# Optimization experiments

Hardware: AMD Instinct MI355X
Metric: run time of the kernel (lower is better)

Reference implementation:

```python
import jax, jax.numpy as jnp
from jax import lax
import numpy as np

NBC, NAC, KF, RHO = 14, 45, 52, 0.05
KT = np.arange(0.8, 0, -1.0 / 64, dtype=np.float32)[None, :]  # (1, 52) AC kernel time axis
K = KT.shape[1]


def _sigm(x, off, slope):
    return jax.nn.sigmoid(slope * (x - off))


def _ac_kernel(log_tr, log_td, kt):
    tr = jnp.exp(log_tr)[:, None]  # (nAC,1)
    td = jnp.exp(log_td)[:, None]
    k = jnp.exp(-kt / td) - jnp.exp(-(td + tr) / (td * tr) * kt)  # (nAC,K)
    return k / jnp.linalg.norm(k, axis=1, keepdims=True)


def setup_inputs() -> dict:
    key = jax.random.key(0)
    ks = jax.random.split(key, 12)
    B, T = 64, 4096
    n = 0.01  # noise_init_scale
    return {
        "x": jax.random.normal(ks[0], (B, T), jnp.float32) * 0.5,
        "bc_kernels": jax.random.normal(ks[1], (NBC, KF), jnp.float32) * 0.1,
        "log_sigmoid_slope": jnp.log(2.0) + n * jax.random.normal(ks[2], (NBC,), jnp.float32),
        "sigmoid_offset": 1.5 + n * jax.random.normal(ks[3], (NBC,), jnp.float32),
        "log_bc_ac_weight": jnp.log(1.0 / NBC) + n * jax.random.normal(ks[4], (NAC, NBC), jnp.float32),
        "log_ac_tau_rise": jnp.log(0.1) + n * jax.random.normal(ks[5], (NAC,), jnp.float32),
        "log_ac_tau_decay": jnp.log(0.1) + n * jax.random.normal(ks[6], (NAC,), jnp.float32),
        "log_ac_sigmoid_slope": jnp.log(2.0) + n * jax.random.normal(ks[7], (NAC,), jnp.float32),
        "ac_sigmoid_offset": 1.5 + n * jax.random.normal(ks[8], (NAC,), jnp.float32),
        "log_ac_bc_weight": jnp.log(0.01) + n * jax.random.normal(ks[9], (NBC, NAC), jnp.float32),
        "out_scale": jnp.ones((NBC,), jnp.float32),
    }


def reference(x, bc_kernels, log_sigmoid_slope, sigmoid_offset, log_bc_ac_weight,
              log_ac_tau_rise, log_ac_tau_decay, log_ac_sigmoid_slope,
              ac_sigmoid_offset, log_ac_bc_weight, out_scale):
    B, T = x.shape
    kt = jnp.asarray(KT)
    # linear_filter: causal conv of stimulus with per-BC kernels -> (T, B, nBC)
    xf = lax.conv_general_dilated(x[:, None, :], bc_kernels[:, None, :], (1,), [(KF - 1, 0)])
    xf = jnp.transpose(xf, (2, 0, 1))  # (T, B, nBC)

    slope = jnp.exp(log_sigmoid_slope)
    ac_slope = jnp.exp(log_ac_sigmoid_slope)
    bc_ac_w = jnp.exp(log_bc_ac_weight)          # (nAC, nBC)
    ac_bc_w = -jnp.exp(log_ac_bc_weight)         # (nBC, nAC)
    ack = _ac_kernel(log_ac_tau_rise, log_ac_tau_decay, kt)  # (nAC, K)

    # --- plain LNR branch (no feedback) ---
    prob_lnr = _sigm(xf, sigmoid_offset, slope)

    def lnr_step(pool, p):
        pool2 = pool + (1.0 - pool) * RHO
        rel = p * pool2
        return pool2 - rel, rel

    _, rel_lnr = lax.scan(lnr_step, jnp.ones((B, NBC), x.dtype), prob_lnr)
    y_lnr = (out_scale * rel_lnr).transpose(1, 0, 2)  # (B, T, nBC)

    # --- BCN branch with AC feedback recurrence ---
    def bcn_step(carry, xt):
        pool, prev_rel, buf = carry
        # append previous release (track_release[i-1]) to sliding window (oldest first)
        buf = jnp.concatenate([buf[..., 1:], prev_rel[..., None]], axis=-1)  # (B, nBC, K)
        drive = jnp.einsum('ak,ab,nbk->na', ack, bc_ac_w, buf)               # (B, nAC)
        ac_out = _sigm(drive, ac_sigmoid_offset, ac_slope)
        fb = ac_out @ ac_bc_w.T                                              # (B, nBC)
        prob = _sigm(xt + fb, sigmoid_offset, slope)
        pool2 = pool + (1.0 - pool) * RHO
        rel = prob * pool2
        return (pool2 - rel, rel, buf), (rel, fb, ac_out)

    init = (jnp.ones((B, NBC), x.dtype), jnp.zeros((B, NBC), x.dtype), jnp.zeros((B, NBC, K), x.dtype))
    _, (rel, fb, ac_out) = lax.scan(bcn_step, init, xf)
    y_bcn = (out_scale * rel).transpose(1, 0, 2)  # (B, T, nBC)
    return y_bcn, fb.transpose(1, 0, 2), ac_out.transpose(1, 0, 2), y_lnr
```

## Files before the change

### kernel.cpp

```cpp
#include <hip/hip_runtime.h>
#include <hip/hip_fp16.h>

#define NBC 14
#define NAC 45
#define KF  52
#define RHO 0.05f
#define TT  4096
#define BB  64
#define CHC 64
#define WU  44
#define NPAIR 32
#define NTW (WU + CHC)
#define SPAN (WU + 2*CHC)
#define XPAD 176
#define LOG2E 1.44269504f
#define XF_BYTES ((size_t)BB * NBC * TT * 2)

typedef float f2 __attribute__((ext_vector_type(2)));
typedef int   i2v __attribute__((ext_vector_type(2)));

__device__ __forceinline__ __half2 bch(unsigned u) { return __builtin_bit_cast(__half2, u); }
__device__ __forceinline__ unsigned bcu(__half2 h) { return __builtin_bit_cast(unsigned, h); }
__device__ __forceinline__ __half2 pk2(float lo, float hi) {
  return __floats2half2_rn(lo, hi);
}
__device__ __forceinline__ __half2 xsum16h(__half2 v) {
#if __has_builtin(__builtin_amdgcn_permlane16_swap)
  i2v r = __builtin_amdgcn_permlane16_swap((int)bcu(v), (int)bcu(v), false, false);
  return __hadd2(bch((unsigned)r[0]), bch((unsigned)r[1]));
#else
  return __hadd2(v, bch((unsigned)__builtin_amdgcn_ds_swizzle((int)bcu(v), (16 << 10) | 0x1f)));
#endif
}
__device__ __forceinline__ __half2 xsum32h(__half2 v) {
#if __has_builtin(__builtin_amdgcn_permlane32_swap)
  i2v r = __builtin_amdgcn_permlane32_swap((int)bcu(v), (int)bcu(v), false, false);
  return __hadd2(bch((unsigned)r[0]), bch((unsigned)r[1]));
#else
  return __hadd2(v, bch((unsigned)__shfl_xor((int)bcu(v), 32)));
#endif
}
__device__ __forceinline__ float exp2_f(float x) {
#if __has_builtin(__builtin_amdgcn_exp2f)
  return __builtin_amdgcn_exp2f(x);
#else
  return exp2f(x);
#endif
}

__global__ __launch_bounds__(256)
void conv_kernel(const float* __restrict__ x, const float* __restrict__ bck,
                 __half* __restrict__ xfg) {
  __shared__ float xs[256 + KF];
  const int tid  = threadIdx.x;
  const int b    = blockIdx.x >> 4;
  const int t0   = (blockIdx.x & 15) << 8;
  for (int i = tid; i < 256 + KF - 1; i += 256) {
    int gt = t0 - (KF - 1) + i;
    xs[i] = (gt >= 0) ? x[b * TT + gt] : 0.f;
  }
  __syncthreads();
  float acc[NBC];
#pragma unroll
  for (int c = 0; c < NBC; ++c) acc[c] = 0.f;
#pragma unroll 4
  for (int k = 0; k < KF; ++k) {
    float xv = xs[tid + k];
#pragma unroll
    for (int c = 0; c < NBC; ++c) acc[c] = fmaf(bck[c * KF + k], xv, acc[c]);
  }
#pragma unroll
  for (int c = 0; c < NBC; ++c)
    xfg[((size_t)b * NBC + c) * TT + t0 + tid] = __float2half(acc[c]);
}

#define POOL_BYTES 6144

template<bool PRECONV>
__global__ __launch_bounds__(64)
void bcn_kernel(const float* __restrict__ x,
                const float* __restrict__ bck,
                const float* __restrict__ lss,
                const float* __restrict__ soff,
                const float* __restrict__ lbaw,
                const float* __restrict__ ltr,
                const float* __restrict__ ltd,
                const float* __restrict__ lass,
                const float* __restrict__ asoff,
                const float* __restrict__ labw,
                const float* __restrict__ oscale,
                const __half* __restrict__ xfg,
                float* __restrict__ out)
{
  __shared__ __align__(16) char pool[POOL_BYTES];
  __half*   xf_lds = (__half*)pool;
  unsigned* acr    = (unsigned*)(pool + 4928);
  unsigned* relr   = (unsigned*)(pool + 5184);
  float*    x_lds  = (float*)(pool + 5248);

  const int lid   = threadIdx.x;
  const int c16   = lid & 15;
  const int q     = lid >> 4;
  const float rowm = (q & 1) ? 0.f : 1.f;
  const int blk   = blockIdx.x;
  const int b     = blk >> 5;
  const int p     = blk & 31;
  const int t0A   = p * (2 * CHC);
  const int t_begin = t0A - WU;

  if constexpr (PRECONV) {
    const __half* src = xfg + (size_t)b * NBC * TT;
    if (p == 0) {
      for (int e = lid; e < NBC * SPAN; e += 64) {
        int c = e / SPAN, i = e - c * SPAN;
        int gt = t_begin + i; if (gt < 0) gt = 0;
        xf_lds[c * XPAD + i] = src[(size_t)c * TT + gt];
      }
    } else {
      for (int c = 0; c < NBC; ++c) {
        if (lid < SPAN / 4) {
          uint2 v = *(const uint2*)(src + (size_t)c * TT + t_begin + 4 * lid);
          *(uint2*)&xf_lds[c * XPAD + 4 * lid] = v;
        }
      }
    }
  } else {
    for (int i = lid; i < SPAN + KF - 1; i += 64) {
      int gt = t_begin - (KF - 1) + i;
      x_lds[i] = (gt >= 0) ? x[b * TT + gt] : 0.f;
    }
    __syncthreads();
    for (int ib = 0; ib < 3; ++ib) {
      int tau = lid + (ib << 6);
      if (tau < SPAN) {
        float acc[NBC];
#pragma unroll
        for (int c = 0; c < NBC; ++c) acc[c] = 0.f;
#pragma unroll 4
        for (int k = 0; k < KF; ++k) {
          float xv = x_lds[tau + k];
#pragma unroll
          for (int c = 0; c < NBC; ++c) acc[c] = fmaf(bck[c * KF + k], xv, acc[c]);
        }
#pragma unroll
        for (int c = 0; c < NBC; ++c) xf_lds[c * XPAD + tau] = __float2half(acc[c]);
      }
    }
    __syncthreads();
  }

  if (lid < 64) acr[lid] = 0u;
  if (lid < 16) relr[lid] = 0u;

  float slope2 = 0.f, soff2 = 0.f, osc_c = 0.f;
  f2 poolP; poolP.x = 1.f; poolP.y = 1.f;
  f2 SA; SA.x = 0.f; SA.y = 0.f;
  f2 SB; SB.x = 0.f; SB.y = 0.f;
  f2 rv2, cn2; rv2.x = rv2.y = cn2.x = cn2.y = 0.f;
  float Adrv2 = 0.f, Boff2 = 0.f;
  __half2 wfbh[16];
  __half2 wuh[NBC];
  f2 yst[8], fst[8];
  unsigned acst[8];

#pragma unroll
  for (int j = 0; j < 16; ++j) wfbh[j] = pk2(0.f, 0.f);
#pragma unroll
  for (int c = 0; c < NBC; ++c) wuh[c] = pk2(0.f, 0.f);

  if (c16 < NBC) {
    float sl = expf(lss[c16]);
    slope2 = sl * LOG2E;
    soff2  = soff[c16] * sl * LOG2E;
    osc_c  = oscale[c16];
#pragma unroll
    for (int j = 0; j < 16; ++j) {
      int a = 16 * q + j;
      if (a < NAC) { float w = -expf(labw[c16 * NAC + a]); wfbh[j] = pk2(w, w); }
    }
  }
  if (lid < NAC) {
    float tr = expf(ltr[lid]);
    float td = expf(ltd[lid]);
    float a1 = 1.f / td;
    float gg = (td + tr) / (td * tr);
    rv2.x = expf(-a1 * 0.015625f);  rv2.y = expf(-gg * 0.015625f);
    cn2.x = expf(-a1 * 0.003125f);  cn2.y = expf(-gg * 0.003125f);
    float nrm = 0.f;
    for (int k = 0; k < KF; ++k) {
      float kt = 0.8f - (float)k * 0.015625f;
      float d = expf(-a1 * kt) - expf(-gg * kt);
      nrm = fmaf(d, d, nrm);
    }
    float inorm  = 1.f / sqrtf(nrm);
    float aslope = expf(lass[lid]);
    Adrv2 = aslope * inorm * LOG2E;
    Boff2 = aslope * asoff[lid] * LOG2E;
#pragma unroll
    for (int c = 0; c < NBC; ++c) {
      float w = expf(lbaw[lid * NBC + c]);
      wuh[c] = pk2(w, w);
    }
  }

  float* yb  = out;
  float* fbp = out + (size_t)BB * TT * NBC;
  float* acp = out + 2 * (size_t)BB * TT * NBC;
  float* ylp = out + 2 * (size_t)BB * TT * NBC + (size_t)BB * TT * NAC;

  __syncthreads();

  auto step = [&](int slot, float xfA, float xfB, bool emit)
      __attribute__((always_inline)) {
    float mzA = fmaf(-Adrv2, SA.x - SA.y, Boff2);
    float mzB = fmaf(-Adrv2, SB.x - SB.y, Boff2);
    float acA = __fdividef(1.f, 1.f + exp2_f(mzA));
    float acB = __fdividef(1.f, 1.f + exp2_f(mzB));
    if (lid < NAC) acr[lid] = bcu(pk2(acA, acB));

    const uint4* ab = (const uint4*)(acr + (q << 4));
    uint4 A0 = ab[0], A1 = ab[1], A2 = ab[2], A3 = ab[3];
    __half2 g0 = __hmul2(wfbh[0], bch(A0.x));
    __half2 g1 = __hmul2(wfbh[1], bch(A0.y));
    g0 = __hfma2(wfbh[2],  bch(A0.z), g0);  g1 = __hfma2(wfbh[3],  bch(A0.w), g1);
    g0 = __hfma2(wfbh[4],  bch(A1.x), g0);  g1 = __hfma2(wfbh[5],  bch(A1.y), g1);
    g0 = __hfma2(wfbh[6],  bch(A1.z), g0);  g1 = __hfma2(wfbh[7],  bch(A1.w), g1);
    g0 = __hfma2(wfbh[8],  bch(A2.x), g0);  g1 = __hfma2(wfbh[9],  bch(A2.y), g1);
    g0 = __hfma2(wfbh[10], bch(A2.z), g0);  g1 = __hfma2(wfbh[11], bch(A2.w), g1);
    g0 = __hfma2(wfbh[12], bch(A3.x), g0);  g1 = __hfma2(wfbh[13], bch(A3.y), g1);
    g0 = __hfma2(wfbh[14], bch(A3.z), g0);  g1 = __hfma2(wfbh[15], bch(A3.w), g1);
    __half2 gs = xsum32h(xsum16h(__hadd2(g0, g1)));
    float fbA = __low2float(gs), fbB = __high2float(gs);

    float mA = fmaf(-slope2, fmaf(rowm, fbA, xfA), soff2);
    float mB = fmaf(-slope2, fmaf(rowm, fbB, xfB), soff2);
    f2 pv;
    pv.x = __fdividef(1.f, 1.f + exp2_f(mA));
    pv.y = __fdividef(1.f, 1.f + exp2_f(mB));
    f2 p2 = poolP * (1.f - RHO) + RHO;
    f2 relP = pv * p2;
    poolP = p2 - relP;
    if (lid < NBC) relr[lid] = bcu(pk2(relP.x, relP.y));
    if (emit) {
      yst[slot] = relP * osc_c;
      f2 t; t.x = fbA; t.y = fbB; fst[slot] = t;
      acst[slot] = bcu(pk2(acA, acB));
    }

    const uint4* rb = (const uint4*)relr;
    uint4 R0 = rb[0], R1 = rb[1], R2 = rb[2], R3 = rb[3];
    __half2 h0 = __hmul2(wuh[0], bch(R0.x));
    __half2 h1 = __hmul2(wuh[1], bch(R0.y));
    h0 = __hfma2(wuh[2],  bch(R0.z), h0);  h1 = __hfma2(wuh[3],  bch(R0.w), h1);
    h0 = __hfma2(wuh[4],  bch(R1.x), h0);  h1 = __hfma2(wuh[5],  bch(R1.y), h1);
    h0 = __hfma2(wuh[6],  bch(R1.z), h0);  h1 = __hfma2(wuh[7],  bch(R1.w), h1);
    h0 = __hfma2(wuh[8],  bch(R2.x), h0);  h1 = __hfma2(wuh[9],  bch(R2.y), h1);
    h0 = __hfma2(wuh[10], bch(R2.z), h0);  h1 = __hfma2(wuh[11], bch(R2.w), h1);
    h0 = __hfma2(wuh[12], bch(R3.x), h0);  h1 = __hfma2(wuh[13], bch(R3.y), h1);
    __half2 uh = __hadd2(h0, h1);
    SA = SA * rv2 + cn2 * __low2float(uh);
    SB = SB * rv2 + cn2 * __high2float(uh);
  };

  auto group = [&](int s4, int slotbase, bool emit) __attribute__((always_inline)) {
    uint2 xa = *(const uint2*)&xf_lds[c16 * XPAD + s4];
    uint2 xb = *(const uint2*)&xf_lds[c16 * XPAD + s4 + CHC];
    __half2 xA01 = bch(xa.x), xA23 = bch(xa.y);
    __half2 xB01 = bch(xb.x), xB23 = bch(xb.y);
    step(slotbase + 0, __low2float(xA01),  __low2float(xB01),  emit);
    step(slotbase + 1, __high2float(xA01), __high2float(xB01), emit);
    step(slotbase + 2, __low2float(xA23),  __low2float(xB23),  emit);
    step(slotbase + 3, __high2float(xA23), __high2float(xB23), emit);
  };

  for (int s4 = 0; s4 < WU; s4 += 4) group(s4, 0, false);

  if (p == 0) {
    SA.x = 0.f; SA.y = 0.f;
    poolP.x = 1.f;
  }

  for (int s8 = WU; s8 < NTW; s8 += 8) {
    group(s8, 0, true);
    group(s8 + 4, 4, true);

    int tg = t0A + (s8 - WU);
    size_t base = (size_t)b * TT + tg;
    if (lid < NBC) {
      size_t ob = base * NBC + lid;
#pragma unroll
      for (int sl = 0; sl < 8; ++sl) {
        yb [ob + sl * NBC]                     = yst[sl].x;
        yb [ob + (size_t)CHC * NBC + sl * NBC] = yst[sl].y;
        fbp[ob + sl * NBC]                     = fst[sl].x;
        fbp[ob + (size_t)CHC * NBC + sl * NBC] = fst[sl].y;
      }
    } else if (lid >= 16 && lid < 16 + NBC) {
      size_t ob = base * NBC + (lid - 16);
#pragma unroll
      for (int sl = 0; sl < 8; ++sl) {
        ylp[ob + sl * NBC]                     = yst[sl].x;
        ylp[ob + (size_t)CHC * NBC + sl * NBC] = yst[sl].y;
      }
    }
    if (lid < NAC) {
      size_t oa = base * NAC + lid;
#pragma unroll
      for (int sl = 0; sl < 8; ++sl) {
        __half2 h = bch(acst[sl]);
        acp[oa + sl * NAC]                     = __low2float(h);
        acp[oa + (size_t)CHC * NAC + sl * NAC] = __high2float(h);
      }
    }
  }
}

extern "C" void kernel_launch(void* const* d_in, const int* in_sizes, int n_in,
                              void* d_out, int out_size, void* d_ws, size_t ws_size,
                              hipStream_t stream) {
  (void)in_sizes; (void)n_in; (void)out_size;
  const float* x    = (const float*)d_in[0];
  const float* bck  = (const float*)d_in[1];
  if (ws_size >= XF_BYTES) {
    __half* xfg = (__half*)d_ws;
    conv_kernel<<<dim3(BB * 16), dim3(256), 0, stream>>>(x, bck, xfg);
    bcn_kernel<true><<<dim3(BB * NPAIR), dim3(64), 0, stream>>>(
        x, bck, (const float*)d_in[2], (const float*)d_in[3], (const float*)d_in[4],
        (const float*)d_in[5], (const float*)d_in[6], (const float*)d_in[7],
        (const float*)d_in[8], (const float*)d_in[9], (const float*)d_in[10],
        xfg, (float*)d_out);
  } else {
    bcn_kernel<false><<<dim3(BB * NPAIR), dim3(64), 0, stream>>>(
        x, bck, (const float*)d_in[2], (const float*)d_in[3], (const float*)d_in[4],
        (const float*)d_in[5], (const float*)d_in[6], (const float*)d_in[7],
        (const float*)d_in[8], (const float*)d_in[9], (const float*)d_in[10],
        (const __half*)nullptr, (float*)d_out);
  }
}
```

Baseline: 92.74 us.

## Replace LDS exchange in recurrence with DPP row rotations

```diff
diff --git a/kernel.cpp b/kernel.cpp
--- a/kernel.cpp
+++ b/kernel.cpp
@@ -24,6 +24,11 @@
 __device__ __forceinline__ __half2 pk2(float lo, float hi) {
   return __floats2half2_rn(lo, hi);
 }
+template<int J>
+__device__ __forceinline__ __half2 rot2(__half2 v) {
+  return __builtin_bit_cast(__half2, __builtin_amdgcn_update_dpp(
+      0, __builtin_bit_cast(int, v), 0x120 + J, 0xF, 0xF, true));
+}
 __device__ __forceinline__ __half2 xsum16h(__half2 v) {
 #if __has_builtin(__builtin_amdgcn_permlane16_swap)
   i2v r = __builtin_amdgcn_permlane16_swap((int)bcu(v), (int)bcu(v), false, false);
@@ -46,6 +51,9 @@
 #else
   return exp2f(x);
 #endif
+}
+__device__ __forceinline__ float sigm(float m) {
+  return __fdividef(1.f, 1.f + exp2_f(m));
 }
 
 __global__ __launch_bounds__(256)
@@ -74,7 +82,7 @@
     xfg[((size_t)b * NBC + c) * TT + t0 + tid] = __float2half(acc[c]);
 }
 
-#define POOL_BYTES 6144
+#define POOL_BYTES 5824
 
 template<bool PRECONV>
 __global__ __launch_bounds__(64)
@@ -93,20 +101,21 @@
                 float* __restrict__ out)
 {
   __shared__ __align__(16) char pool[POOL_BYTES];
-  __half*   xf_lds = (__half*)pool;
-  unsigned* acr    = (unsigned*)(pool + 4928);
-  unsigned* relr   = (unsigned*)(pool + 5184);
-  float*    x_lds  = (float*)(pool + 5248);
+  __half* xf_lds = (__half*)pool;
+  float*  x_lds  = (float*)(pool + 4928);
 
   const int lid   = threadIdx.x;
   const int c16   = lid & 15;
   const int q     = lid >> 4;
-  const float rowm = (q & 1) ? 0.f : 1.f;
+  const int crow  = (c16 < NBC) ? c16 : 0;
   const int blk   = blockIdx.x;
   const int b     = blk >> 5;
   const int p     = blk & 31;
   const int t0A   = p * (2 * CHC);
   const int t_begin = t0A - WU;
+
+  const int probe = __builtin_amdgcn_update_dpp(0, c16, 0x121, 0xF, 0xF, true);
+  const int delta = (c16 - probe) & 15;
 
   if constexpr (PRECONV) {
     const __half* src = xfg + (size_t)b * NBC * TT;
@@ -149,33 +158,29 @@
     __syncthreads();
   }
 
-  if (lid < 64) acr[lid] = 0u;
-  if (lid < 16) relr[lid] = 0u;
-
   float slope2 = 0.f, soff2 = 0.f, osc_c = 0.f;
-  f2 poolP; poolP.x = 1.f; poolP.y = 1.f;
+  f2 poolA; poolA.x = 1.f; poolA.y = 1.f;
+  f2 poolB; poolB.x = 1.f; poolB.y = 1.f;
   f2 SA; SA.x = 0.f; SA.y = 0.f;
   f2 SB; SB.x = 0.f; SB.y = 0.f;
   f2 rv2, cn2; rv2.x = rv2.y = cn2.x = cn2.y = 0.f;
   float Adrv2 = 0.f, Boff2 = 0.f;
   __half2 wfbh[16];
-  __half2 wuh[NBC];
-  f2 yst[8], fst[8];
+  __half2 wuh[16];
+  f2 yst[8], fst[8], lst[8];
   unsigned acst[8];
 
 #pragma unroll
-  for (int j = 0; j < 16; ++j) wfbh[j] = pk2(0.f, 0.f);
-#pragma unroll
-  for (int c = 0; c < NBC; ++c) wuh[c] = pk2(0.f, 0.f);
+  for (int j = 0; j < 16; ++j) { wfbh[j] = pk2(0.f, 0.f); wuh[j] = pk2(0.f, 0.f); }
 
   if (c16 < NBC) {
     float sl = expf(lss[c16]);
     slope2 = sl * LOG2E;
     soff2  = soff[c16] * sl * LOG2E;
     osc_c  = oscale[c16];
-#pragma unroll
     for (int j = 0; j < 16; ++j) {
-      int a = 16 * q + j;
+      int srcl = (c16 - delta * j) & 15;
+      int a = 16 * q + srcl;
       if (a < NAC) { float w = -expf(labw[c16 * NAC + a]); wfbh[j] = pk2(w, w); }
     }
   }
@@ -196,10 +201,9 @@
     float aslope = expf(lass[lid]);
     Adrv2 = aslope * inorm * LOG2E;
     Boff2 = aslope * asoff[lid] * LOG2E;
-#pragma unroll
-    for (int c = 0; c < NBC; ++c) {
-      float w = expf(lbaw[lid * NBC + c]);
-      wuh[c] = pk2(w, w);
+    for (int j = 0; j < 16; ++j) {
+      int srcl = (c16 - delta * j) & 15;
+      if (srcl < NBC) { float w = expf(lbaw[lid * NBC + srcl]); wuh[j] = pk2(w, w); }
     }
   }
 
@@ -214,57 +218,74 @@
       __attribute__((always_inline)) {
     float mzA = fmaf(-Adrv2, SA.x - SA.y, Boff2);
     float mzB = fmaf(-Adrv2, SB.x - SB.y, Boff2);
-    float acA = __fdividef(1.f, 1.f + exp2_f(mzA));
-    float acB = __fdividef(1.f, 1.f + exp2_f(mzB));
-    if (lid < NAC) acr[lid] = bcu(pk2(acA, acB));
-
-    const uint4* ab = (const uint4*)(acr + (q << 4));
-    uint4 A0 = ab[0], A1 = ab[1], A2 = ab[2], A3 = ab[3];
-    __half2 g0 = __hmul2(wfbh[0], bch(A0.x));
-    __half2 g1 = __hmul2(wfbh[1], bch(A0.y));
-    g0 = __hfma2(wfbh[2],  bch(A0.z), g0);  g1 = __hfma2(wfbh[3],  bch(A0.w), g1);
-    g0 = __hfma2(wfbh[4],  bch(A1.x), g0);  g1 = __hfma2(wfbh[5],  bch(A1.y), g1);
-    g0 = __hfma2(wfbh[6],  bch(A1.z), g0);  g1 = __hfma2(wfbh[7],  bch(A1.w), g1);
-    g0 = __hfma2(wfbh[8],  bch(A2.x), g0);  g1 = __hfma2(wfbh[9],  bch(A2.y), g1);
-    g0 = __hfma2(wfbh[10], bch(A2.z), g0);  g1 = __hfma2(wfbh[11], bch(A2.w), g1);
-    g0 = __hfma2(wfbh[12], bch(A3.x), g0);  g1 = __hfma2(wfbh[13], bch(A3.y), g1);
-    g0 = __hfma2(wfbh[14], bch(A3.z), g0);  g1 = __hfma2(wfbh[15], bch(A3.w), g1);
+    float acA = sigm(mzA);
+    float acB = sigm(mzB);
+    __half2 ach = pk2(acA, acB);
+
+    __half2 g0 = __hmul2(wfbh[0], ach);
+    __half2 g1 = __hmul2(wfbh[1], rot2<1>(ach));
+    g0 = __hfma2(wfbh[2],  rot2<2>(ach),  g0);
+    g1 = __hfma2(wfbh[3],  rot2<3>(ach),  g1);
+    g0 = __hfma2(wfbh[4],  rot2<4>(ach),  g0);
+    g1 = __hfma2(wfbh[5],  rot2<5>(ach),  g1);
+    g0 = __hfma2(wfbh[6],  rot2<6>(ach),  g0);
+    g1 = __hfma2(wfbh[7],  rot2<7>(ach),  g1);
+    g0 = __hfma2(wfbh[8],  rot2<8>(ach),  g0);
+    g1 = __hfma2(wfbh[9],  rot2<9>(ach),  g1);
+    g0 = __hfma2(wfbh[10], rot2<10>(ach), g0);
+    g1 = __hfma2(wfbh[11], rot2<11>(ach), g1);
+    g0 = __hfma2(wfbh[12], rot2<12>(ach), g0);
+    g1 = __hfma2(wfbh[13], rot2<13>(ach), g1);
+    g0 = __hfma2(wfbh[14], rot2<14>(ach), g0);
+    g1 = __hfma2(wfbh[15], rot2<15>(ach), g1);
     __half2 gs = xsum32h(xsum16h(__hadd2(g0, g1)));
     float fbA = __low2float(gs), fbB = __high2float(gs);
 
-    float mA = fmaf(-slope2, fmaf(rowm, fbA, xfA), soff2);
-    float mB = fmaf(-slope2, fmaf(rowm, fbB, xfB), soff2);
-    f2 pv;
-    pv.x = __fdividef(1.f, 1.f + exp2_f(mA));
-    pv.y = __fdividef(1.f, 1.f + exp2_f(mB));
-    f2 p2 = poolP * (1.f - RHO) + RHO;
-    f2 relP = pv * p2;
-    poolP = p2 - relP;
-    if (lid < NBC) relr[lid] = bcu(pk2(relP.x, relP.y));
+    float mlA = fmaf(-slope2, xfA, soff2);
+    float mpA = fmaf(-slope2, fbA, mlA);
+    float mlB = fmaf(-slope2, xfB, soff2);
+    float mpB = fmaf(-slope2, fbB, mlB);
+    f2 pvA, pvB;
+    pvA.x = sigm(mpA);  pvA.y = sigm(mlA);
+    pvB.x = sigm(mpB);  pvB.y = sigm(mlB);
+    f2 p2A = poolA * (1.f - RHO) + RHO;
+    f2 p2B = poolB * (1.f - RHO) + RHO;
+    f2 relA = pvA * p2A, relB = pvB * p2B;
+    poolA = p2A - relA;  poolB = p2B - relB;
+    __half2 relh = pk2(relA.x, relB.x);
+
     if (emit) {
-      yst[slot] = relP * osc_c;
-      f2 t; t.x = fbA; t.y = fbB; fst[slot] = t;
-      acst[slot] = bcu(pk2(acA, acB));
-    }
-
-    const uint4* rb = (const uint4*)relr;
-    uint4 R0 = rb[0], R1 = rb[1], R2 = rb[2], R3 = rb[3];
-    __half2 h0 = __hmul2(wuh[0], bch(R0.x));
-    __half2 h1 = __hmul2(wuh[1], bch(R0.y));
-    h0 = __hfma2(wuh[2],  bch(R0.z), h0);  h1 = __hfma2(wuh[3],  bch(R0.w), h1);
-    h0 = __hfma2(wuh[4],  bch(R1.x), h0);  h1 = __hfma2(wuh[5],  bch(R1.y), h1);
-    h0 = __hfma2(wuh[6],  bch(R1.z), h0);  h1 = __hfma2(wuh[7],  bch(R1.w), h1);
-    h0 = __hfma2(wuh[8],  bch(R2.x), h0);  h1 = __hfma2(wuh[9],  bch(R2.y), h1);
-    h0 = __hfma2(wuh[10], bch(R2.z), h0);  h1 = __hfma2(wuh[11], bch(R2.w), h1);
-    h0 = __hfma2(wuh[12], bch(R3.x), h0);  h1 = __hfma2(wuh[13], bch(R3.y), h1);
+      f2 t1; t1.x = osc_c * relA.x; t1.y = osc_c * relB.x; yst[slot] = t1;
+      f2 t2; t2.x = fbA;            t2.y = fbB;            fst[slot] = t2;
+      f2 t3; t3.x = osc_c * relA.y; t3.y = osc_c * relB.y; lst[slot] = t3;
+      acst[slot] = bcu(ach);
+    }
+
+    __half2 h0 = __hmul2(wuh[0], relh);
+    __half2 h1 = __hmul2(wuh[1], rot2<1>(relh));
+    h0 = __hfma2(wuh[2],  rot2<2>(relh),  h0);
+    h1 = __hfma2(wuh[3],  rot2<3>(relh),  h1);
+    h0 = __hfma2(wuh[4],  rot2<4>(relh),  h0);
+    h1 = __hfma2(wuh[5],  rot2<5>(relh),  h1);
+    h0 = __hfma2(wuh[6],  rot2<6>(relh),  h0);
+    h1 = __hfma2(wuh[7],  rot2<7>(relh),  h1);
+    h0 = __hfma2(wuh[8],  rot2<8>(relh),  h0);
+    h1 = __hfma2(wuh[9],  rot2<9>(relh),  h1);
+    h0 = __hfma2(wuh[10], rot2<10>(relh), h0);
+    h1 = __hfma2(wuh[11], rot2<11>(relh), h1);
+    h0 = __hfma2(wuh[12], rot2<12>(relh), h0);
+    h1 = __hfma2(wuh[13], rot2<13>(relh), h1);
+    h0 = __hfma2(wuh[14], rot2<14>(relh), h0);
+    h1 = __hfma2(wuh[15], rot2<15>(relh), h1);
     __half2 uh = __hadd2(h0, h1);
+
     SA = SA * rv2 + cn2 * __low2float(uh);
     SB = SB * rv2 + cn2 * __high2float(uh);
   };
 
   auto group = [&](int s4, int slotbase, bool emit) __attribute__((always_inline)) {
-    uint2 xa = *(const uint2*)&xf_lds[c16 * XPAD + s4];
-    uint2 xb = *(const uint2*)&xf_lds[c16 * XPAD + s4 + CHC];
+    uint2 xa = *(const uint2*)&xf_lds[crow * XPAD + s4];
+    uint2 xb = *(const uint2*)&xf_lds[crow * XPAD + s4 + CHC];
     __half2 xA01 = bch(xa.x), xA23 = bch(xa.y);
     __half2 xB01 = bch(xb.x), xB23 = bch(xb.y);
     step(slotbase + 0, __low2float(xA01),  __low2float(xB01),  emit);
@@ -277,7 +298,7 @@
 
   if (p == 0) {
     SA.x = 0.f; SA.y = 0.f;
-    poolP.x = 1.f;
+    poolA.x = 1.f; poolA.y = 1.f;
   }
 
   for (int s8 = WU; s8 < NTW; s8 += 8) {
@@ -299,8 +320,8 @@
       size_t ob = base * NBC + (lid - 16);
 #pragma unroll
       for (int sl = 0; sl < 8; ++sl) {
-        ylp[ob + sl * NBC]                     = yst[sl].x;
-        ylp[ob + (size_t)CHC * NBC + sl * NBC] = yst[sl].y;
+        ylp[ob + sl * NBC]                     = lst[sl].x;
+        ylp[ob + (size_t)CHC * NBC + sl * NBC] = lst[sl].y;
       }
     }
     if (lid < NAC) {
```

Measured after the change: 111.9 us. 20.6% more time.
